# Performance work log

Hardware: AMD Instinct MI355X
Metric: run time of the kernel (lower is better)

Reference implementation:

```python
import jax, jax.numpy as jnp
import numpy as np

N = 300000   # total atoms
E = 600000   # directed edges
G = 8192     # molecules in batch
D = 6        # node_feat_dim
H = 128      # hidden_dim
OUT = 256    # embedding_dim
L = 4        # num GIN layers


def setup_inputs() -> dict:
    key = jax.random.key(0)
    ks = jax.random.split(key, 12)
    s_in = 1.0 / np.sqrt(D)
    s_h = 1.0 / np.sqrt(H)
    return {
        "x": jax.random.normal(ks[0], (N, D), jnp.float32),
        "edge_index": jax.random.randint(ks[1], (2, E), 0, N, dtype=jnp.int32),
        "batch": jnp.sort(jax.random.randint(ks[2], (N,), 0, G, dtype=jnp.int32)),
        "W_enc": jax.random.normal(ks[3], (D, H), jnp.float32) * s_in,
        "b_enc": jnp.zeros((H,), jnp.float32),
        "W1": jax.random.normal(ks[4], (L, H, H), jnp.float32) * s_h,
        "b1": jnp.zeros((L, H), jnp.float32),
        "W2": jax.random.normal(ks[5], (L, H, H), jnp.float32) * s_h,
        "b2": jnp.zeros((L, H), jnp.float32),
        "W_out": jax.random.normal(ks[6], (H, OUT), jnp.float32) * s_h,
        "b_out": jnp.zeros((OUT,), jnp.float32),
    }


def reference(x, edge_index, batch, W_enc, b_enc, W1, b1, W2, b2, W_out, b_out):
    n = x.shape[0]
    src, dst = edge_index[0], edge_index[1]
    # node encoder
    h = x @ W_enc + b_enc                                   # [N, H]
    # stacked GINConv: out = mlp((1+eps)*x + sum_neighbors), eps = 0
    for l in range(L):
        agg = jax.ops.segment_sum(h[src], dst, num_segments=n)  # gather + scatter-add
        z = h + agg
        z = jax.nn.relu(z @ W1[l] + b1[l]) @ W2[l] + b2[l]      # GIN MLP
        h = jax.nn.relu(z)                                       # outer F.relu
    # global mean pool over graphs
    sums = jax.ops.segment_sum(h, batch, num_segments=G)        # [G, H]
    counts = jax.ops.segment_sum(jnp.ones((n, 1), h.dtype), batch, num_segments=G)
    pooled = sums / jnp.maximum(counts, 1.0)
    return pooled @ W_out + b_out                                # [G, OUT]
```

## Files before the change

kernel.cpp:

```cpp
#include <hip/hip_runtime.h>

#define HD 128

typedef unsigned short ushort_t;
typedef __attribute__((ext_vector_type(8))) unsigned short us8;
typedef __attribute__((ext_vector_type(8))) short s8b;
typedef __attribute__((ext_vector_type(16))) float f32x16;

__device__ __forceinline__ float b2f(unsigned short u) {
    union { unsigned int i; float f; } v; v.i = ((unsigned int)u) << 16; return v.f;
}
__device__ __forceinline__ unsigned short f2b(float f) {
    union { float f; unsigned int i; } v; v.f = f;
    unsigned int u = v.i;
    return (unsigned short)((u + 0x7fffu + ((u >> 16) & 1u)) >> 16);
}

__device__ __forceinline__ void load8f(const float* p, float* o) {
    float4 a = *reinterpret_cast<const float4*>(p);
    float4 b = *reinterpret_cast<const float4*>(p + 4);
    o[0]=a.x;o[1]=a.y;o[2]=a.z;o[3]=a.w;o[4]=b.x;o[5]=b.y;o[6]=b.z;o[7]=b.w;
}
__device__ __forceinline__ void load8b(const ushort_t* p, float* o) {
    us8 v = *reinterpret_cast<const us8*>(p);
#pragma unroll
    for (int j = 0; j < 8; ++j) o[j] = b2f(v[j]);
}
__device__ __forceinline__ void store8b(ushort_t* p, const float* s) {
    us8 v;
#pragma unroll
    for (int j = 0; j < 8; ++j) v[j] = f2b(s[j]);
    *reinterpret_cast<us8*>(p) = v;
}

__device__ __forceinline__ void store1(float* p, float v) { *p = v; }
__device__ __forceinline__ void store1(ushort_t* p, float v) { *p = f2b(v); }

__device__ __forceinline__ int lowerb(const int* __restrict__ a, int n, int v) {
    int lo = 0, hi = n;
    while (lo < hi) { int m = (lo + hi) >> 1; if (a[m] < v) lo = m + 1; else hi = m; }
    return lo;
}

__global__ void hist_kernel(const int* __restrict__ dst, int* __restrict__ deg, int e) {
    int i = blockIdx.x * blockDim.x + threadIdx.x;
    if (i < e) atomicAdd(&deg[dst[i]], 1);
}

#define SCAN_NT 256
#define SCAN_BPT 8
#define SCAN_CHUNK (SCAN_NT * SCAN_BPT)

__global__ __launch_bounds__(SCAN_NT) void scan_a(const int* __restrict__ deg,
                                                  int* __restrict__ bsum, int n) {
    int tid = threadIdx.x;
    int base = blockIdx.x * SCAN_CHUNK + tid * SCAN_BPT;
    int sum = 0;
    if (base + SCAN_BPT <= n) {
        int4 v0 = *reinterpret_cast<const int4*>(deg + base);
        int4 v1 = *reinterpret_cast<const int4*>(deg + base + 4);
        sum = v0.x + v0.y + v0.z + v0.w + v1.x + v1.y + v1.z + v1.w;
    } else {
        for (int j = 0; j < SCAN_BPT; ++j) { int i = base + j; if (i < n) sum += deg[i]; }
    }
    __shared__ int sd[SCAN_NT];
    sd[tid] = sum; __syncthreads();
    for (int off = SCAN_NT / 2; off > 0; off >>= 1) {
        if (tid < off) sd[tid] += sd[tid + off];
        __syncthreads();
    }
    if (tid == 0) bsum[blockIdx.x] = sd[0];
}

__global__ __launch_bounds__(1024) void scan_b(int* __restrict__ bsum, int nb) {
    __shared__ int ps[1024];
    int tid = threadIdx.x;
    int v = (tid < nb) ? bsum[tid] : 0;
    ps[tid] = v; __syncthreads();
    for (int off = 1; off < 1024; off <<= 1) {
        int t = (tid >= off) ? ps[tid - off] : 0;
        __syncthreads();
        ps[tid] += t;
        __syncthreads();
    }
    if (tid < nb) bsum[tid] = ps[tid] - v;
}

__global__ __launch_bounds__(SCAN_NT) void scan_c(const int* __restrict__ deg,
                                                  const int* __restrict__ bsum,
                                                  int* __restrict__ rowptr,
                                                  int* __restrict__ cursor,
                                                  int n, int etot) {
    int tid = threadIdx.x;
    int base = blockIdx.x * SCAN_CHUNK + tid * SCAN_BPT;
    int vals[SCAN_BPT];
    if (base + SCAN_BPT <= n) {
        int4 v0 = *reinterpret_cast<const int4*>(deg + base);
        int4 v1 = *reinterpret_cast<const int4*>(deg + base + 4);
        vals[0]=v0.x; vals[1]=v0.y; vals[2]=v0.z; vals[3]=v0.w;
        vals[4]=v1.x; vals[5]=v1.y; vals[6]=v1.z; vals[7]=v1.w;
    } else {
        for (int j = 0; j < SCAN_BPT; ++j) { int i = base + j; vals[j] = (i < n) ? deg[i] : 0; }
    }
    int sum = 0;
#pragma unroll
    for (int j = 0; j < SCAN_BPT; ++j) sum += vals[j];
    __shared__ int ps[SCAN_NT];
    ps[tid] = sum; __syncthreads();
    for (int off = 1; off < SCAN_NT; off <<= 1) {
        int t = (tid >= off) ? ps[tid - off] : 0;
        __syncthreads();
        ps[tid] += t;
        __syncthreads();
    }
    int run = bsum[blockIdx.x] + ps[tid] - sum;
#pragma unroll
    for (int j = 0; j < SCAN_BPT; ++j) {
        int i = base + j;
        if (i < n) { rowptr[i] = run; cursor[i] = run; run += vals[j]; }
    }
    if (blockIdx.x == 0 && tid == 0) rowptr[n] = etot;
}

__global__ void fill_kernel(const int* __restrict__ src, const int* __restrict__ dst,
                            int* __restrict__ cursor, int* __restrict__ col, int e) {
    int i = blockIdx.x * blockDim.x + threadIdx.x;
    if (i < e) { int slot = atomicAdd(&cursor[dst[i]], 1); col[slot] = src[i]; }
}

__global__ void pack_kernel(const float* __restrict__ W, ushort_t* __restrict__ Wp,
                            int nmat, int ld, int mat_stride, int col_off) {
    int idx = blockIdx.x * blockDim.x + threadIdx.x;
    if (idx >= nmat * 2048) return;
    int lane = idx & 63;
    int ks = (idx >> 6) & 7;
    int j = (idx >> 9) & 3;
    int mat = idx >> 11;
    const float* Wm = W + (size_t)mat * mat_stride;
    int k0 = ks * 16 + (lane >> 5) * 8;
    int n = mat * col_off + j * 32 + (lane & 31);
    us8 o;
#pragma unroll
    for (int e = 0; e < 8; ++e) o[e] = f2b(Wm[(size_t)(k0 + e) * ld + n]);
    *reinterpret_cast<us8*>(Wp + (size_t)idx * 8) = o;
}

__global__ void xagg_kernel(const float* __restrict__ x, const int* __restrict__ rowptr,
                            const int* __restrict__ col, float* __restrict__ xa, int n) {
    int node = blockIdx.x * blockDim.x + threadIdx.x;
    if (node >= n) return;
    const float2* xr = reinterpret_cast<const float2*>(x + (size_t)node * 6);
    float2 a0 = xr[0], a1 = xr[1], a2 = xr[2];
    int lo = rowptr[node], hi = rowptr[node + 1];
    for (int i = lo; i < hi; ++i) {
        const float2* xs = reinterpret_cast<const float2*>(x + (size_t)col[i] * 6);
        float2 s0 = xs[0], s1 = xs[1], s2 = xs[2];
        a0.x += s0.x; a0.y += s0.y; a1.x += s1.x; a1.y += s1.y; a2.x += s2.x; a2.y += s2.y;
    }
    float cnt = (float)(1 + hi - lo);
    float4 o0; o0.x = a0.x; o0.y = a0.y; o0.z = a1.x; o0.w = a1.y;
    float4 o1; o1.x = a2.x; o1.y = a2.y; o1.z = cnt; o1.w = 0.f;
    reinterpret_cast<float4*>(xa + (size_t)node * 8)[0] = o0;
    reinterpret_cast<float4*>(xa + (size_t)node * 8)[1] = o1;
}

__global__ void enc2_kernel(const float* __restrict__ xa, const float* __restrict__ W,
                            const float* __restrict__ b, ushort_t* __restrict__ z, int n) {
    int t = blockIdx.x * blockDim.x + threadIdx.x;
    int q = t >> 4, g = t & 15;
    int node0 = q * 4;
    if (node0 >= n) return;
    float w[6][8];
#pragma unroll
    for (int d = 0; d < 6; ++d) load8f(W + d * HD + g * 8, w[d]);
    float bias[8];
    load8f(b + g * 8, bias);
#pragma unroll
    for (int u = 0; u < 4; ++u) {
        int node = node0 + u;
        if (node >= n) break;
        float4 a0 = reinterpret_cast<const float4*>(xa + (size_t)node * 8)[0];
        float4 a1 = reinterpret_cast<const float4*>(xa + (size_t)node * 8)[1];
        float xv[6] = {a0.x, a0.y, a0.z, a0.w, a1.x, a1.y};
        float cnt = a1.z;
        float acc[8];
#pragma unroll
        for (int j = 0; j < 8; ++j) acc[j] = cnt * bias[j];
#pragma unroll
        for (int d = 0; d < 6; ++d)
#pragma unroll
            for (int j = 0; j < 8; ++j) acc[j] += xv[d] * w[d][j];
        store8b(z + (size_t)node * HD + g * 8, acc);
    }
}

__global__ void agg_kernel(const ushort_t* __restrict__ h, const int* __restrict__ rowptr,
                           const int* __restrict__ col, ushort_t* __restrict__ z, int n) {
    int t = blockIdx.x * blockDim.x + threadIdx.x;
    int node = t >> 4;
    if (node >= n) return;
    int g = t & 15;
    float acc[8];
    load8b(h + (size_t)node * HD + g * 8, acc);
    int lo = rowptr[node], hi = rowptr[node + 1];
    for (int i = lo; i < hi; ++i) {
        int s = col[i];
        float v[8];
        load8b(h + (size_t)s * HD + g * 8, v);
#pragma unroll
        for (int j = 0; j < 8; ++j) acc[j] += v[j];
    }
    store8b(z + (size_t)node * HD + g * 8, acc);
}

__global__ __launch_bounds__(512, 4) void mlp_fused(
    ushort_t* __restrict__ z,
    const ushort_t* __restrict__ Wp1, const ushort_t* __restrict__ Wp2,
    const float* __restrict__ b1, const float* __restrict__ b2)
{
    __shared__ s8b sW1[2048];
    __shared__ s8b sW2[2048];

    const int tid = threadIdx.x;
    for (int i = tid; i < 2048; i += 512) {
        sW1[i] = reinterpret_cast<const s8b*>(Wp1)[i];
        sW2[i] = reinterpret_cast<const s8b*>(Wp2)[i];
    }
    __syncthreads();

    const int lane = tid & 63;
    const int r32  = lane & 31;
    const int h    = lane >> 5;
    const int row0 = blockIdx.x * 256 + (tid >> 6) * 32;
    const int arow = row0 + r32;
    const int koff = h * 8;

    s8b bz[8];
#pragma unroll
    for (int ks = 0; ks < 8; ++ks)
        bz[ks] = *reinterpret_cast<const s8b*>(z + (size_t)arow * HD + ks * 16 + koff);

    s8b a2[8];
#pragma unroll
    for (int j = 0; j < 4; ++j) {
        f32x16 c;
#pragma unroll
        for (int i = 0; i < 16; ++i) c[i] = 0.f;
#pragma unroll
        for (int ks = 0; ks < 8; ++ks)
            c = __builtin_amdgcn_mfma_f32_32x32x16_bf16(sW1[(j * 8 + ks) * 64 + lane], bz[ks], c, 0, 0, 0);
        unsigned int w[4][2];
#pragma unroll
        for (int b = 0; b < 4; ++b) {
            float4 bv = *reinterpret_cast<const float4*>(b1 + j * 32 + b * 8 + 4 * h);
            float v0 = fmaxf(c[4 * b + 0] + bv.x, 0.f);
            float v1 = fmaxf(c[4 * b + 1] + bv.y, 0.f);
            float v2 = fmaxf(c[4 * b + 2] + bv.z, 0.f);
            float v3 = fmaxf(c[4 * b + 3] + bv.w, 0.f);
            w[b][0] = (unsigned int)f2b(v0) | ((unsigned int)f2b(v1) << 16);
            w[b][1] = (unsigned int)f2b(v2) | ((unsigned int)f2b(v3) << 16);
        }
        unsigned int p[4][2];
#pragma unroll
        for (int b = 0; b < 4; ++b) {
            p[b][0] = (unsigned int)__shfl_xor((int)w[b][0], 32);
            p[b][1] = (unsigned int)__shfl_xor((int)w[b][1], 32);
        }
        union { unsigned int u[4]; s8b v; } t0, t1;
        t0.u[0] = (h == 0) ? w[0][0] : p[1][0];
        t0.u[1] = (h == 0) ? w[0][1] : p[1][1];
        t0.u[2] = (h == 0) ? p[0][0] : w[1][0];
        t0.u[3] = (h == 0) ? p[0][1] : w[1][1];
        t1.u[0] = (h == 0) ? w[2][0] : p[3][0];
        t1.u[1] = (h == 0) ? w[2][1] : p[3][1];
        t1.u[2] = (h == 0) ? p[2][0] : w[3][0];
        t1.u[3] = (h == 0) ? p[2][1] : w[3][1];
        a2[2 * j]     = t0.v;
        a2[2 * j + 1] = t1.v;
    }

#pragma unroll
    for (int j = 0; j < 4; ++j) {
        f32x16 c;
#pragma unroll
        for (int i = 0; i < 16; ++i) c[i] = 0.f;
#pragma unroll
        for (int ks = 0; ks < 8; ++ks)
            c = __builtin_amdgcn_mfma_f32_32x32x16_bf16(a2[ks], sW2[(j * 8 + ks) * 64 + lane], c, 0, 0, 0);
        const int ccol = j * 32 + r32;
        const float bv = b2[ccol];
        const int rbase = row0 + 4 * h;
#pragma unroll
        for (int reg = 0; reg < 16; ++reg) {
            int row = rbase + (reg & 3) + 8 * (reg >> 2);
            z[(size_t)row * HD + ccol] = f2b(fmaxf(c[reg] + bv, 0.f));
        }
    }
}

template<typename TO, bool RELU>
__global__ __launch_bounds__(256) void gemm_mfma(
    const ushort_t* __restrict__ A, const ushort_t* __restrict__ Wp,
    const float* __restrict__ bias, TO* __restrict__ out, int ldo)
{
    __shared__ s8b sW[2048];
    const int tid = threadIdx.x;
    for (int i = tid; i < 2048; i += 256)
        sW[i] = reinterpret_cast<const s8b*>(Wp)[i];
    __syncthreads();

    const int lane = tid & 63;
    const int row0 = blockIdx.x * 128 + (tid >> 6) * 32;
    const int arow = row0 + (lane & 31);
    const int koff = (lane >> 5) * 8;

    s8b a[8];
#pragma unroll
    for (int ks = 0; ks < 8; ++ks)
        a[ks] = *reinterpret_cast<const s8b*>(A + (size_t)arow * HD + ks * 16 + koff);

#pragma unroll
    for (int j = 0; j < 4; ++j) {
        f32x16 acc;
#pragma unroll
        for (int i = 0; i < 16; ++i) acc[i] = 0.f;
#pragma unroll
        for (int ks = 0; ks < 8; ++ks)
            acc = __builtin_amdgcn_mfma_f32_32x32x16_bf16(a[ks], sW[(j * 8 + ks) * 64 + lane], acc, 0, 0, 0);
        const int col = j * 32 + (lane & 31);
        const float bv = bias[col];
        const int rbase = row0 + 4 * (lane >> 5);
#pragma unroll
        for (int reg = 0; reg < 16; ++reg) {
            int row = rbase + (reg & 3) + 8 * (reg >> 2);
            float v = acc[reg] + bv;
            if (RELU) v = fmaxf(v, 0.f);
            store1(out + (size_t)row * ldo + col, v);
        }
    }
}

__global__ __launch_bounds__(128) void pool_kernel(const ushort_t* __restrict__ h,
                                                   const int* __restrict__ batch,
                                                   ushort_t* __restrict__ pooled, int n) {
    int g = blockIdx.x;
    int c = threadIdx.x;
    int start = lowerb(batch, n, g);
    int end = lowerb(batch, n, g + 1);
    float s = 0.f;
    for (int i = start; i < end; ++i) s += b2f(h[(size_t)i * HD + c]);
    int cnt = end - start; if (cnt < 1) cnt = 1;
    pooled[(size_t)g * HD + c] = f2b(s / (float)cnt);
}

extern "C" void kernel_launch(void* const* d_in, const int* in_sizes, int n_in,
                              void* d_out, int out_size, void* d_ws, size_t ws_size,
                              hipStream_t stream) {
    const float* x      = (const float*)d_in[0];
    const int*   edge   = (const int*)d_in[1];
    const int*   batch  = (const int*)d_in[2];
    const float* W_enc  = (const float*)d_in[3];
    const float* b_enc  = (const float*)d_in[4];
    const float* W1     = (const float*)d_in[5];
    const float* b1     = (const float*)d_in[6];
    const float* W2     = (const float*)d_in[7];
    const float* b2     = (const float*)d_in[8];
    const float* W_out  = (const float*)d_in[9];
    const float* b_out  = (const float*)d_in[10];

    const int N = in_sizes[0] / 6;
    const int E = in_sizes[1] / 2;
    const int G = out_size / 256;
    const int L = in_sizes[5] / (HD * HD);
    const int Npad = ((N + 255) / 256) * 256;

    const int* srcv = edge;
    const int* dstv = edge + E;

    size_t off = 0;
    auto alloc = [&](size_t bytes) -> char* {
        char* p = (char*)d_ws + off;
        off += (bytes + 255) & ~(size_t)255;
        return p;
    };
    ushort_t* bufA   = (ushort_t*)alloc((size_t)Npad * HD * 2);
    ushort_t* bufB   = (ushort_t*)alloc((size_t)Npad * HD * 2);
    ushort_t* pooled = (ushort_t*)alloc((size_t)G * HD * 2);
    ushort_t* Wp1    = (ushort_t*)alloc((size_t)L * 16384 * 2);
    ushort_t* Wp2    = (ushort_t*)alloc((size_t)L * 16384 * 2);
    ushort_t* WpO    = (ushort_t*)alloc((size_t)2 * 16384 * 2);
    float* xaggb = (float*)alloc((size_t)N * 8 * 4);
    int* rowptr = (int*)alloc((size_t)(N + 1) * 4);
    int* cursor = (int*)alloc((size_t)N * 4);
    int* colidx = (int*)alloc((size_t)E * 4);
    int* deg    = (int*)alloc((size_t)N * 4);
    int* bsum   = (int*)alloc((size_t)1024 * 4);
    (void)ws_size;

    const int nb = (N + SCAN_CHUNK - 1) / SCAN_CHUNK;
    hipMemsetAsync(deg, 0, (size_t)N * 4, stream);
    hist_kernel<<<(E + 255) / 256, 256, 0, stream>>>(dstv, deg, E);
    scan_a<<<nb, SCAN_NT, 0, stream>>>(deg, bsum, N);
    scan_b<<<1, 1024, 0, stream>>>(bsum, nb);
    scan_c<<<nb, SCAN_NT, 0, stream>>>(deg, bsum, rowptr, cursor, N, E);
    fill_kernel<<<(E + 255) / 256, 256, 0, stream>>>(srcv, dstv, cursor, colidx, E);

    pack_kernel<<<(L * 2048 + 255) / 256, 256, 0, stream>>>(W1, Wp1, L, HD, HD * HD, 0);
    pack_kernel<<<(L * 2048 + 255) / 256, 256, 0, stream>>>(W2, Wp2, L, HD, HD * HD, 0);
    pack_kernel<<<(2 * 2048 + 255) / 256, 256, 0, stream>>>(W_out, WpO, 2, 256, 0, 128);

    xagg_kernel<<<(N + 255) / 256, 256, 0, stream>>>(x, rowptr, colidx, xaggb, N);
    {
        int threads = ((N + 3) / 4) * 16;
        enc2_kernel<<<(threads + 255) / 256, 256, 0, stream>>>(xaggb, W_enc, b_enc, bufA, N);
    }
    const int nblk = Npad / 256;
    mlp_fused<<<nblk, 512, 0, stream>>>(bufA, Wp1, Wp2, b1, b2);

    ushort_t* cur = bufA;
    ushort_t* oth = bufB;
    for (int l = 1; l < L; ++l) {
        agg_kernel<<<(N * 16 + 255) / 256, 256, 0, stream>>>(cur, rowptr, colidx, oth, N);
        mlp_fused<<<nblk, 512, 0, stream>>>(
            oth, Wp1 + (size_t)l * 16384, Wp2 + (size_t)l * 16384,
            b1 + (size_t)l * HD, b2 + (size_t)l * HD);
        ushort_t* t = cur; cur = oth; oth = t;
    }

    pool_kernel<<<G, 128, 0, stream>>>(cur, batch, pooled, N);

    float* outp = (float*)d_out;
    gemm_mfma<float, false><<<G / 128, 256, 0, stream>>>(pooled, WpO, b_out, outp, 256);
    gemm_mfma<float, false><<<G / 128, 256, 0, stream>>>(pooled, WpO + 16384, b_out + 128, outp + 128, 256);
}
```

Before: 466.8 us.

## Fuse neighbor aggregation into the GIN MLP kernel for layers 1-3

Replaces the separate aggregation kernel plus MLP kernel with one kernel per layer. Each lane gathers its node's row and its neighbors' rows directly into MFMA operand registers, then runs both GEMMs and writes the next layer's hidden state. This removes the intermediate z write and read round trip and one launch per layer. In exchange, each lane now gathers whole 64-element half-rows serially, so the gather parallelism drops and register pressure rises (a 64-float accumulator) under launch bounds of 512 threads by 4 blocks. That could reduce occupancy or cause spills.

Result: no change. 464.4 us (-0.5%).

```diff
diff --git a/kernel.cpp b/kernel.cpp
--- a/kernel.cpp
+++ b/kernel.cpp
@@ -194,25 +194,6 @@
     }
 }
 
-__global__ void agg_kernel(const ushort_t* __restrict__ h, const int* __restrict__ rowptr,
-                           const int* __restrict__ col, ushort_t* __restrict__ z, int n) {
-    int t = blockIdx.x * blockDim.x + threadIdx.x;
-    int node = t >> 4;
-    if (node >= n) return;
-    int g = t & 15;
-    float acc[8];
-    load8b(h + (size_t)node * HD + g * 8, acc);
-    int lo = rowptr[node], hi = rowptr[node + 1];
-    for (int i = lo; i < hi; ++i) {
-        int s = col[i];
-        float v[8];
-        load8b(h + (size_t)s * HD + g * 8, v);
-#pragma unroll
-        for (int j = 0; j < 8; ++j) acc[j] += v[j];
-    }
-    store8b(z + (size_t)node * HD + g * 8, acc);
-}
-
 __global__ __launch_bounds__(512, 4) void mlp_fused(
     ushort_t* __restrict__ z,
     const ushort_t* __restrict__ Wp1, const ushort_t* __restrict__ Wp2,
@@ -294,6 +275,121 @@
         for (int reg = 0; reg < 16; ++reg) {
             int row = rbase + (reg & 3) + 8 * (reg >> 2);
             z[(size_t)row * HD + ccol] = f2b(fmaxf(c[reg] + bv, 0.f));
+        }
+    }
+}
+
+__global__ __launch_bounds__(512, 4) void gin_layer(
+    const ushort_t* __restrict__ hin, const int* __restrict__ rowptr,
+    const int* __restrict__ col,
+    const ushort_t* __restrict__ Wp1, const ushort_t* __restrict__ Wp2,
+    const float* __restrict__ b1, const float* __restrict__ b2,
+    ushort_t* __restrict__ hout, int n)
+{
+    __shared__ s8b sW1[2048];
+    __shared__ s8b sW2[2048];
+
+    const int tid = threadIdx.x;
+    for (int i = tid; i < 2048; i += 512) {
+        sW1[i] = reinterpret_cast<const s8b*>(Wp1)[i];
+        sW2[i] = reinterpret_cast<const s8b*>(Wp2)[i];
+    }
+    __syncthreads();
+
+    const int lane = tid & 63;
+    const int r32  = lane & 31;
+    const int h    = lane >> 5;
+    const int row0 = blockIdx.x * 256 + (tid >> 6) * 32;
+    const int arow = row0 + r32;
+    const int koff = h * 8;
+
+    s8b bz[8];
+    {
+        float facc[8][8];
+        if (arow < n) {
+            const ushort_t* hr = hin + (size_t)arow * HD + koff;
+#pragma unroll
+            for (int ks = 0; ks < 8; ++ks) {
+                us8 v = *reinterpret_cast<const us8*>(hr + ks * 16);
+#pragma unroll
+                for (int e = 0; e < 8; ++e) facc[ks][e] = b2f(v[e]);
+            }
+            const int lo = rowptr[arow], hi = rowptr[arow + 1];
+            for (int i = lo; i < hi; ++i) {
+                const ushort_t* hs = hin + (size_t)col[i] * HD + koff;
+#pragma unroll
+                for (int ks = 0; ks < 8; ++ks) {
+                    us8 v = *reinterpret_cast<const us8*>(hs + ks * 16);
+#pragma unroll
+                    for (int e = 0; e < 8; ++e) facc[ks][e] += b2f(v[e]);
+                }
+            }
+        } else {
+#pragma unroll
+            for (int ks = 0; ks < 8; ++ks)
+#pragma unroll
+                for (int e = 0; e < 8; ++e) facc[ks][e] = 0.f;
+        }
+#pragma unroll
+        for (int ks = 0; ks < 8; ++ks)
+#pragma unroll
+            for (int e = 0; e < 8; ++e) bz[ks][e] = (short)f2b(facc[ks][e]);
+    }
+
+    s8b a2[8];
+#pragma unroll
+    for (int j = 0; j < 4; ++j) {
+        f32x16 c;
+#pragma unroll
+        for (int i = 0; i < 16; ++i) c[i] = 0.f;
+#pragma unroll
+        for (int ks = 0; ks < 8; ++ks)
+            c = __builtin_amdgcn_mfma_f32_32x32x16_bf16(sW1[(j * 8 + ks) * 64 + lane], bz[ks], c, 0, 0, 0);
+        unsigned int w[4][2];
+#pragma unroll
+        for (int b = 0; b < 4; ++b) {
+            float4 bv = *reinterpret_cast<const float4*>(b1 + j * 32 + b * 8 + 4 * h);
+            float v0 = fmaxf(c[4 * b + 0] + bv.x, 0.f);
+            float v1 = fmaxf(c[4 * b + 1] + bv.y, 0.f);
+            float v2 = fmaxf(c[4 * b + 2] + bv.z, 0.f);
+            float v3 = fmaxf(c[4 * b + 3] + bv.w, 0.f);
+            w[b][0] = (unsigned int)f2b(v0) | ((unsigned int)f2b(v1) << 16);
+            w[b][1] = (unsigned int)f2b(v2) | ((unsigned int)f2b(v3) << 16);
+        }
+        unsigned int p[4][2];
+#pragma unroll
+        for (int b = 0; b < 4; ++b) {
+            p[b][0] = (unsigned int)__shfl_xor((int)w[b][0], 32);
+            p[b][1] = (unsigned int)__shfl_xor((int)w[b][1], 32);
+        }
+        union { unsigned int u[4]; s8b v; } t0, t1;
+        t0.u[0] = (h == 0) ? w[0][0] : p[1][0];
+        t0.u[1] = (h == 0) ? w[0][1] : p[1][1];
+        t0.u[2] = (h == 0) ? p[0][0] : w[1][0];
+        t0.u[3] = (h == 0) ? p[0][1] : w[1][1];
+        t1.u[0] = (h == 0) ? w[2][0] : p[3][0];
+        t1.u[1] = (h == 0) ? w[2][1] : p[3][1];
+        t1.u[2] = (h == 0) ? p[2][0] : w[3][0];
+        t1.u[3] = (h == 0) ? p[2][1] : w[3][1];
+        a2[2 * j]     = t0.v;
+        a2[2 * j + 1] = t1.v;
+    }
+
+#pragma unroll
+    for (int j = 0; j < 4; ++j) {
+        f32x16 c;
+#pragma unroll
+        for (int i = 0; i < 16; ++i) c[i] = 0.f;
+#pragma unroll
+        for (int ks = 0; ks < 8; ++ks)
+            c = __builtin_amdgcn_mfma_f32_32x32x16_bf16(a2[ks], sW2[(j * 8 + ks) * 64 + lane], c, 0, 0, 0);
+        const int ccol = j * 32 + r32;
+        const float bv = b2[ccol];
+        const int rbase = row0 + 4 * h;
+#pragma unroll
+        for (int reg = 0; reg < 16; ++reg) {
+            int row = rbase + (reg & 3) + 8 * (reg >> 2);
+            hout[(size_t)row * HD + ccol] = f2b(fmaxf(c[reg] + bv, 0.f));
         }
     }
 }
@@ -420,10 +516,10 @@
     ushort_t* cur = bufA;
     ushort_t* oth = bufB;
     for (int l = 1; l < L; ++l) {
-        agg_kernel<<<(N * 16 + 255) / 256, 256, 0, stream>>>(cur, rowptr, colidx, oth, N);
-        mlp_fused<<<nblk, 512, 0, stream>>>(
-            oth, Wp1 + (size_t)l * 16384, Wp2 + (size_t)l * 16384,
-            b1 + (size_t)l * HD, b2 + (size_t)l * HD);
+        gin_layer<<<nblk, 512, 0, stream>>>(
+            cur, rowptr, colidx,
+            Wp1 + (size_t)l * 16384, Wp2 + (size_t)l * 16384,
+            b1 + (size_t)l * HD, b2 + (size_t)l * HD, oth, N);
         ushort_t* t = cur; cur = oth; oth = t;
     }
 
```
